# Kernel tuning notes

Measured on AMD Instinct MI355X. Metric: run time of the kernel, lower is better.

The kernel has to match this reference:

```python
import jax, jax.numpy as jnp
import numpy as np

NUM_EMB = 1000
HIDDEN = 256
SCALE = 2
N_HEADS = 8
HEAD_DIM = HIDDEN * SCALE // N_HEADS  # 64
HS = HIDDEN * SCALE  # 512
EPS = 1e-6


def setup_inputs() -> dict:
    key = jax.random.key(0)
    ks = jax.random.split(key, 12)
    B, N, C, H, W = 8, 8, HIDDEN, 32, 32
    std = 0.02
    return {
        "q": jax.random.randint(ks[0], (B,), 0, NUM_EMB, dtype=jnp.int32),
        "c": jax.random.normal(ks[1], (B, N, C, H, W), dtype=jnp.float32),
        "rms_w": jnp.ones((HIDDEN,), dtype=jnp.float32),
        "emb": jax.random.normal(ks[2], (NUM_EMB, HIDDEN), dtype=jnp.float32) * std,
        "w1": jax.random.normal(ks[3], (HIDDEN, HS), dtype=jnp.float32) * std,
        "b1": jnp.zeros((HS,), dtype=jnp.float32),
        "w2": jax.random.normal(ks[4], (HS, HS), dtype=jnp.float32) * std,
        "b2": jnp.zeros((HS,), dtype=jnp.float32),
        "w_kv": jax.random.normal(ks[5], (HIDDEN, HS * 2), dtype=jnp.float32) * std,
        "w_out": jax.random.normal(ks[6], (HS, HIDDEN), dtype=jnp.float32) * std,
        "b_out": jnp.zeros((HIDDEN,), dtype=jnp.float32),
    }


def reference(q, c, rms_w, emb, w1, b1, w2, b2, w_kv, w_out, b_out):
    B, N, C, H, W = c.shape
    attn_scale = HEAD_DIM ** (-0.5)
    # permute to [B,H,W,N,C] and RMSNorm over channel dim
    c = jnp.transpose(c, (0, 3, 4, 1, 2))
    c = c * jax.lax.rsqrt(jnp.mean(c * c, axis=-1, keepdims=True) + EPS) * rms_w
    # query path: embed + gated MLP -> [B, n_heads, head_dim]
    qe = emb[q]                                   # [B, hidden]
    qh = jax.nn.silu(qe @ w1 + b1) @ w2 + b2      # [B, HS]
    qh = qh.reshape(B, N_HEADS, HEAD_DIM)
    # kv projection: [B,H,W,N, 2*HS] -> [B,H,W,n_heads,N, 2*head_dim]
    kv = (c @ w_kv).reshape(B, H, W, N, N_HEADS, 2 * HEAD_DIM)
    kv = jnp.transpose(kv, (0, 1, 2, 4, 3, 5))
    k, v = jnp.split(kv, 2, axis=-1)              # each [B,H,W,heads,N,head_dim]
    # broadcast per-pixel cross-attention: query shared over H,W
    dots = jnp.einsum('bed,bhwend->bhwen', qh, k) * attn_scale
    attn = jax.nn.softmax(dots, axis=-1)
    h = jnp.einsum('bhwen,bhwend->bhwed', attn, v)  # [B,H,W,heads,head_dim]
    h = h.reshape(B, H, W, HS)
    out = h @ w_out + b_out                        # [B,H,W,hidden]
    return jnp.transpose(out, (0, 3, 1, 2))        # [B,hidden,H,W]
```

## Files before the change

### kernel.cpp

```cpp
#include <hip/hip_runtime.h>

typedef _Float16 f16;
typedef _Float16 f16x4 __attribute__((ext_vector_type(4)));
typedef _Float16 f16x8 __attribute__((ext_vector_type(8)));
typedef float f32x4 __attribute__((ext_vector_type(4)));

static __device__ inline char* a_addr(char* Abase, int px, int k) {
    return Abase + px * 4096 + ((((k >> 3) ^ (px & 15)) << 4) | ((k & 7) << 1));
}

__launch_bounds__(256)
__global__ void k_setup(const int* __restrict__ q, const float* __restrict__ emb,
                        const float* __restrict__ w1, const float* __restrict__ b1,
                        const float* __restrict__ w2, const float* __restrict__ b2,
                        const float* __restrict__ w_kv, const float* __restrict__ w_out,
                        const float* __restrict__ rms_w,
                        f16* __restrict__ qkw, f16* __restrict__ mtp) {
    int blk = blockIdx.x;
    int t = threadIdx.x;
    __shared__ float qe[256];
    __shared__ float x1L[512];
    __shared__ float ps[4][64];
    __shared__ float qhL[64];
    __shared__ float wv[64][8];

    if (blk < 64) {
        int b = blk >> 3, e = blk & 7;
        qe[t] = emb[(size_t)q[b] * 256 + t];
        __syncthreads();
        float a0 = b1[t], a1 = b1[t + 256];
#pragma unroll 4
        for (int c = 0; c < 256; ++c) {
            float qv = qe[c];
            a0 += qv * w1[c * 512 + t];
            a1 += qv * w1[c * 512 + t + 256];
        }
        x1L[t]       = a0 / (1.f + __expf(-a0));
        x1L[t + 256] = a1 / (1.f + __expf(-a1));
        __syncthreads();
        int d = t & 63, ks = t >> 6;
        float acc = 0.f;
#pragma unroll 4
        for (int k = ks * 128; k < ks * 128 + 128; ++k)
            acc += x1L[k] * w2[k * 512 + e * 64 + d];
        ps[ks][d] = acc;
        __syncthreads();
        if (t < 64)
            qhL[t] = b2[e * 64 + t] + ps[0][t] + ps[1][t] + ps[2][t] + ps[3][t];
        __syncthreads();
        const float* row = w_kv + (size_t)t * 1024 + e * 128;
        float a2 = 0.f;
#pragma unroll
        for (int dd = 0; dd < 64; dd += 4) {
            float4 wv4 = *(const float4*)(row + dd);
            a2 += qhL[dd] * wv4.x + qhL[dd + 1] * wv4.y + qhL[dd + 2] * wv4.z + qhL[dd + 3] * wv4.w;
        }
        qkw[(b * 8 + e) * 256 + t] = (f16)(a2 * rms_w[t]);
    } else {
        int mb = blk - 64;
        int e = mb >> 5, c0 = (mb & 31) * 8;
        {
            int d = t & 63, cc = t >> 6;
            wv[d][cc]     = w_kv[(size_t)(c0 + cc) * 1024 + e * 128 + 64 + d];
            wv[d][cc + 4] = w_kv[(size_t)(c0 + cc + 4) * 1024 + e * 128 + 64 + d];
        }
        __syncthreads();
        int o = t;
        float acc[8];
#pragma unroll
        for (int c = 0; c < 8; ++c) acc[c] = 0.f;
#pragma unroll 4
        for (int d = 0; d < 64; ++d) {
            float wo = w_out[(size_t)(e * 64 + d) * 256 + o];
            float4 wa = *(const float4*)&wv[d][0];
            float4 wb = *(const float4*)&wv[d][4];
            acc[0] += wa.x * wo; acc[1] += wa.y * wo; acc[2] += wa.z * wo; acc[3] += wa.w * wo;
            acc[4] += wb.x * wo; acc[5] += wb.y * wo; acc[6] += wb.z * wo; acc[7] += wb.w * wo;
        }
        f16x8 ov;
#pragma unroll
        for (int c = 0; c < 8; ++c) ov[c] = (f16)(acc[c] * rms_w[c0 + c]);
        *(f16x8*)(mtp + ((size_t)((e * 256 + c0) >> 3) * 256 + o) * 8) = ov;
    }
}

__launch_bounds__(1024, 8)
__global__ void k_attn(const float* __restrict__ cin, const f16* __restrict__ qkw,
                       const f16* __restrict__ mtp, const float* __restrict__ b_out,
                       float* __restrict__ out) {
    int blk = blockIdx.x;
    int b = blk & 7;
    int hw0 = (blk >> 3) * 16;
    int t = threadIdx.x;
    int lane = t & 63, w = t >> 6;
    int m16 = lane & 15, quad = lane >> 4;

    __shared__ char A[16 * 4096];
    __shared__ float dotsP[8][8][16];
    __shared__ float wred[16][16];
    __shared__ float rinvL[16][9];

    {
        int px = m16;
        int cb = (w << 2) | quad;
        const float* src = cin + ((size_t)b * 2048 + (size_t)cb * 32) * 1024 + hw0 + px;
        float ss = 0.f;
#pragma unroll
        for (int jb = 0; jb < 4; jb += 2) {
            float v0[8], v1[8];
#pragma unroll
            for (int j = 0; j < 8; ++j) v0[j] = src[(size_t)(jb * 8 + j) << 10];
#pragma unroll
            for (int j = 0; j < 8; ++j) v1[j] = src[(size_t)(jb * 8 + 8 + j) << 10];
            f16x8 h0, h1;
#pragma unroll
            for (int j = 0; j < 8; ++j) { ss += v0[j] * v0[j]; h0[j] = (f16)v0[j]; }
#pragma unroll
            for (int j = 0; j < 8; ++j) { ss += v1[j] * v1[j]; h1[j] = (f16)v1[j]; }
            *(f16x8*)a_addr(A, px, cb * 32 + jb * 8)     = h0;
            *(f16x8*)a_addr(A, px, cb * 32 + jb * 8 + 8) = h1;
        }
        ss += __shfl_xor(ss, 16);
        ss += __shfl_xor(ss, 32);
        if (lane < 16) wred[w][lane] = ss;
    }
    __syncthreads();

    if (w < 8) {
        int n = w;
        f32x4 d0 = {0.f, 0.f, 0.f, 0.f};
        const f16* qrow = qkw + (size_t)b * 2048 + (m16 & 7) * 256;
#pragma unroll
        for (int ks = 0; ks < 8; ++ks) {
            f16x8 a0 = *(const f16x8*)a_addr(A, m16, n * 256 + ks * 32 + quad * 8);
            f16x8 bq = *(const f16x8*)(qrow + ks * 32 + quad * 8);
            d0 = __builtin_amdgcn_mfma_f32_16x16x32_f16(a0, bq, d0, 0, 0, 0);
        }
        if (m16 < 8) {
#pragma unroll
            for (int r = 0; r < 4; ++r) dotsP[n][m16][quad * 4 + r] = d0[r];
        }
    } else if (w < 10) {
        int i = t - 512;
        int p = i & 15, n = i >> 4;
        float ss = wred[2 * n][p] + wred[2 * n + 1][p];
        rinvL[p][n] = rsqrtf(ss * (1.f / 256.f) + 1e-6f);
    }
    __syncthreads();

    {
        int bpx = t & 15;
        int cw = t >> 4;
        float rinv[8];
#pragma unroll
        for (int n = 0; n < 8; ++n) rinv[n] = rinvL[bpx][n];
        f16x4 cv[8];
#pragma unroll
        for (int n = 0; n < 8; ++n)
            cv[n] = *(const f16x4*)a_addr(A, bpx, n * 256 + cw * 4);
#pragma unroll
        for (int e = 0; e < 8; ++e) {
            float l[8];
#pragma unroll
            for (int n = 0; n < 8; ++n) l[n] = dotsP[n][e][bpx] * rinv[n] * 0.125f;
            float mx = l[0];
#pragma unroll
            for (int n = 1; n < 8; ++n) mx = fmaxf(mx, l[n]);
            float s = 0.f;
#pragma unroll
            for (int n = 0; n < 8; ++n) { l[n] = __expf(l[n] - mx); s += l[n]; }
            float inv = 1.f / s;
            f16x4 r = {};
#pragma unroll
            for (int n = 0; n < 8; ++n) {
                f16 an = (f16)(l[n] * inv * rinv[n]);
#pragma unroll
                for (int j = 0; j < 4; ++j) r[j] += cv[n][j] * an;
            }
            *(f16x4*)a_addr(A, bpx, e * 256 + cw * 4) = r;
        }
    }
    __syncthreads();

    {
        int o = (w << 4) | m16;
        float bo = b_out[o];
        f32x4 acc = {0.f, 0.f, 0.f, 0.f};
#pragma unroll 4
        for (int ks = 0; ks < 64; ++ks) {
            int k = ks * 32 + quad * 8;
            f16x8 bfr = *(const f16x8*)(mtp + ((size_t)(ks * 4 + quad) * 256 + o) * 8);
            f16x8 af  = *(const f16x8*)a_addr(A, m16, k);
            acc = __builtin_amdgcn_mfma_f32_16x16x32_f16(af, bfr, acc, 0, 0, 0);
        }
        float* drow = out + ((size_t)b * 256 + o) * 1024 + hw0;
        float4 v0 = {acc[0] + bo, acc[1] + bo, acc[2] + bo, acc[3] + bo};
        *(float4*)(drow + quad * 4) = v0;
    }
}

extern "C" void kernel_launch(void* const* d_in, const int* in_sizes, int n_in,
                              void* d_out, int out_size, void* d_ws, size_t ws_size,
                              hipStream_t stream) {
    (void)in_sizes; (void)n_in; (void)out_size; (void)ws_size;
    const int*   q     = (const int*)d_in[0];
    const float* c     = (const float*)d_in[1];
    const float* rms_w = (const float*)d_in[2];
    const float* emb   = (const float*)d_in[3];
    const float* w1    = (const float*)d_in[4];
    const float* b1    = (const float*)d_in[5];
    const float* w2    = (const float*)d_in[6];
    const float* b2    = (const float*)d_in[7];
    const float* w_kv  = (const float*)d_in[8];
    const float* w_out = (const float*)d_in[9];
    const float* b_out = (const float*)d_in[10];
    float* out = (float*)d_out;

    char* ws = (char*)d_ws;
    f16* qkw = (f16*)ws;
    f16* mtp = (f16*)(ws + 32768);

    k_setup<<<320, 256, 0, stream>>>(q, emb, w1, b1, w2, b2, w_kv, w_out, rms_w, qkw, mtp);
    k_attn <<<512, 1024, 0, stream>>>(c, qkw, mtp, b_out, out);
}
```

Baseline: 178.2 us.

## Process two pixel tiles per attention block and restructure setup kernel

```diff
diff --git a/kernel.cpp b/kernel.cpp
--- a/kernel.cpp
+++ b/kernel.cpp
@@ -9,7 +9,7 @@
     return Abase + px * 4096 + ((((k >> 3) ^ (px & 15)) << 4) | ((k & 7) << 1));
 }
 
-__launch_bounds__(256)
+__launch_bounds__(1024)
 __global__ void k_setup(const int* __restrict__ q, const float* __restrict__ emb,
                         const float* __restrict__ w1, const float* __restrict__ b1,
                         const float* __restrict__ w2, const float* __restrict__ b2,
@@ -18,64 +18,98 @@
                         f16* __restrict__ qkw, f16* __restrict__ mtp) {
     int blk = blockIdx.x;
     int t = threadIdx.x;
-    __shared__ float qe[256];
-    __shared__ float x1L[512];
-    __shared__ float ps[4][64];
-    __shared__ float qhL[64];
-    __shared__ float wv[64][8];
-
-    if (blk < 64) {
-        int b = blk >> 3, e = blk & 7;
-        qe[t] = emb[(size_t)q[b] * 256 + t];
-        __syncthreads();
-        float a0 = b1[t], a1 = b1[t + 256];
+
+    if (blk == 0) {
+        __shared__ float qeL[8][256];
+        __shared__ float x1L[8][512];
+        __shared__ float qhL[8][512];
+        {
+            int bb = t >> 8, c = t & 255;
+            qeL[bb][c]     = emb[(size_t)q[bb] * 256 + c];
+            qeL[bb + 4][c] = emb[(size_t)q[bb + 4] * 256 + c];
+        }
+        __syncthreads();
+        {
+            int bb = t >> 7, hq = t & 127;
+            float4 bv = *(const float4*)(b1 + hq * 4);
+            f32x4 acc = {bv.x, bv.y, bv.z, bv.w};
+#pragma unroll 8
+            for (int c = 0; c < 256; ++c) {
+                float4 wr = *(const float4*)(w1 + (size_t)c * 512 + hq * 4);
+                float qv = qeL[bb][c];
+                acc[0] += qv * wr.x; acc[1] += qv * wr.y;
+                acc[2] += qv * wr.z; acc[3] += qv * wr.w;
+            }
+#pragma unroll
+            for (int j = 0; j < 4; ++j) {
+                float a = acc[j];
+                x1L[bb][hq * 4 + j] = a / (1.f + __expf(-a));
+            }
+        }
+        __syncthreads();
+        {
+            int bb = t >> 7, oq = t & 127;
+            float4 bv = *(const float4*)(b2 + oq * 4);
+            f32x4 acc = {bv.x, bv.y, bv.z, bv.w};
+#pragma unroll 8
+            for (int k = 0; k < 512; ++k) {
+                float4 wr = *(const float4*)(w2 + (size_t)k * 512 + oq * 4);
+                float xv = x1L[bb][k];
+                acc[0] += xv * wr.x; acc[1] += xv * wr.y;
+                acc[2] += xv * wr.z; acc[3] += xv * wr.w;
+            }
+#pragma unroll
+            for (int j = 0; j < 4; ++j) qhL[bb][oq * 4 + j] = acc[j];
+        }
+        __syncthreads();
+        {
+            int c = t & 255;
+            float rw = rms_w[c];
+#pragma unroll
+            for (int e2 = 0; e2 < 2; ++e2) {
+                int e = (t >> 8) * 2 + e2;
+                const float* col = w_kv + (size_t)c * 1024 + e * 128;
+                float acc[8] = {0.f, 0.f, 0.f, 0.f, 0.f, 0.f, 0.f, 0.f};
 #pragma unroll 4
-        for (int c = 0; c < 256; ++c) {
-            float qv = qe[c];
-            a0 += qv * w1[c * 512 + t];
-            a1 += qv * w1[c * 512 + t + 256];
-        }
-        x1L[t]       = a0 / (1.f + __expf(-a0));
-        x1L[t + 256] = a1 / (1.f + __expf(-a1));
-        __syncthreads();
-        int d = t & 63, ks = t >> 6;
-        float acc = 0.f;
-#pragma unroll 4
-        for (int k = ks * 128; k < ks * 128 + 128; ++k)
-            acc += x1L[k] * w2[k * 512 + e * 64 + d];
-        ps[ks][d] = acc;
-        __syncthreads();
-        if (t < 64)
-            qhL[t] = b2[e * 64 + t] + ps[0][t] + ps[1][t] + ps[2][t] + ps[3][t];
-        __syncthreads();
-        const float* row = w_kv + (size_t)t * 1024 + e * 128;
-        float a2 = 0.f;
-#pragma unroll
-        for (int dd = 0; dd < 64; dd += 4) {
-            float4 wv4 = *(const float4*)(row + dd);
-            a2 += qhL[dd] * wv4.x + qhL[dd + 1] * wv4.y + qhL[dd + 2] * wv4.z + qhL[dd + 3] * wv4.w;
-        }
-        qkw[(b * 8 + e) * 256 + t] = (f16)(a2 * rms_w[t]);
+                for (int dq = 0; dq < 16; ++dq) {
+                    float4 wv4 = *(const float4*)(col + dq * 4);
+#pragma unroll
+                    for (int bb = 0; bb < 8; ++bb) {
+                        const float* qb = &qhL[bb][e * 64 + dq * 4];
+                        acc[bb] += wv4.x * qb[0] + wv4.y * qb[1]
+                                 + wv4.z * qb[2] + wv4.w * qb[3];
+                    }
+                }
+#pragma unroll
+                for (int bb = 0; bb < 8; ++bb)
+                    qkw[(bb * 8 + e) * 256 + c] = (f16)(acc[bb] * rw);
+            }
+        }
     } else {
-        int mb = blk - 64;
+        __shared__ float wv[4][64][8];
+        int sub = t >> 8, st = t & 255;
+        int mb = (blk - 1) * 4 + sub;
         int e = mb >> 5, c0 = (mb & 31) * 8;
-        {
-            int d = t & 63, cc = t >> 6;
-            wv[d][cc]     = w_kv[(size_t)(c0 + cc) * 1024 + e * 128 + 64 + d];
-            wv[d][cc + 4] = w_kv[(size_t)(c0 + cc + 4) * 1024 + e * 128 + 64 + d];
-        }
-        __syncthreads();
-        int o = t;
+        int o = st;
+        float wo[64];
+#pragma unroll
+        for (int d = 0; d < 64; ++d) wo[d] = w_out[(size_t)(e * 64 + d) * 256 + o];
+        {
+            int d = st & 63, cc = st >> 6;
+            wv[sub][d][cc]     = w_kv[(size_t)(c0 + cc) * 1024 + e * 128 + 64 + d];
+            wv[sub][d][cc + 4] = w_kv[(size_t)(c0 + cc + 4) * 1024 + e * 128 + 64 + d];
+        }
+        __syncthreads();
         float acc[8];
 #pragma unroll
         for (int c = 0; c < 8; ++c) acc[c] = 0.f;
-#pragma unroll 4
+#pragma unroll 8
         for (int d = 0; d < 64; ++d) {
-            float wo = w_out[(size_t)(e * 64 + d) * 256 + o];
-            float4 wa = *(const float4*)&wv[d][0];
-            float4 wb = *(const float4*)&wv[d][4];
-            acc[0] += wa.x * wo; acc[1] += wa.y * wo; acc[2] += wa.z * wo; acc[3] += wa.w * wo;
-            acc[4] += wb.x * wo; acc[5] += wb.y * wo; acc[6] += wb.z * wo; acc[7] += wb.w * wo;
+            float w = wo[d];
+            float4 wa = *(const float4*)&wv[sub][d][0];
+            float4 wb = *(const float4*)&wv[sub][d][4];
+            acc[0] += wa.x * w; acc[1] += wa.y * w; acc[2] += wa.z * w; acc[3] += wa.w * w;
+            acc[4] += wb.x * w; acc[5] += wb.y * w; acc[6] += wb.z * w; acc[7] += wb.w * w;
         }
         f16x8 ov;
 #pragma unroll
@@ -84,118 +118,154 @@
     }
 }
 
-__launch_bounds__(1024, 8)
+static __device__ inline void dots_rinv(char* A, const f16* qkw_b,
+                                        float (*dotsP)[8][16], float (*wred)[16],
+                                        float (*rinvL)[9],
+                                        int t, int w, int m16, int quad) {
+    if (w < 8) {
+        int n = w;
+        f32x4 d0 = {0.f, 0.f, 0.f, 0.f};
+        const f16* qrow = qkw_b + (m16 & 7) * 256;
+#pragma unroll
+        for (int ks = 0; ks < 8; ++ks) {
+            f16x8 a0 = *(const f16x8*)a_addr(A, m16, n * 256 + ks * 32 + quad * 8);
+            f16x8 bq = *(const f16x8*)(qrow + ks * 32 + quad * 8);
+            d0 = __builtin_amdgcn_mfma_f32_16x16x32_f16(a0, bq, d0, 0, 0, 0);
+        }
+        if (m16 < 8) {
+#pragma unroll
+            for (int r = 0; r < 4; ++r) dotsP[n][m16][quad * 4 + r] = d0[r];
+        }
+    } else if (w < 10) {
+        int i = t - 512;
+        int p = i & 15, n = i >> 4;
+        float ss = wred[2 * n][p] + wred[2 * n + 1][p];
+        rinvL[p][n] = rsqrtf(ss * (1.f / 256.f) + 1e-6f);
+    }
+}
+
+static __device__ inline void blend(char* A, float (*dotsP)[8][16],
+                                    float (*rinvL)[9], int t) {
+    int bpx = t & 15;
+    int cw = t >> 4;
+    float rinv[8];
+#pragma unroll
+    for (int n = 0; n < 8; ++n) rinv[n] = rinvL[bpx][n];
+    f16x4 cv[8];
+#pragma unroll
+    for (int n = 0; n < 8; ++n)
+        cv[n] = *(const f16x4*)a_addr(A, bpx, n * 256 + cw * 4);
+#pragma unroll
+    for (int e = 0; e < 8; ++e) {
+        float l[8];
+#pragma unroll
+        for (int n = 0; n < 8; ++n) l[n] = dotsP[n][e][bpx] * rinv[n] * 0.125f;
+        float mx = l[0];
+#pragma unroll
+        for (int n = 1; n < 8; ++n) mx = fmaxf(mx, l[n]);
+        float s = 0.f;
+#pragma unroll
+        for (int n = 0; n < 8; ++n) { l[n] = __expf(l[n] - mx); s += l[n]; }
+        float inv = 1.f / s;
+        f16x4 r = {};
+#pragma unroll
+        for (int n = 0; n < 8; ++n) {
+            f16 an = (f16)(l[n] * inv * rinv[n]);
+#pragma unroll
+            for (int j = 0; j < 4; ++j) r[j] += cv[n][j] * an;
+        }
+        *(f16x4*)a_addr(A, bpx, e * 256 + cw * 4) = r;
+    }
+}
+
+__launch_bounds__(1024, 4)
 __global__ void k_attn(const float* __restrict__ cin, const f16* __restrict__ qkw,
                        const f16* __restrict__ mtp, const float* __restrict__ b_out,
                        float* __restrict__ out) {
     int blk = blockIdx.x;
     int b = blk & 7;
-    int hw0 = (blk >> 3) * 16;
+    int hw0 = (blk >> 3) * 32;
     int t = threadIdx.x;
     int lane = t & 63, w = t >> 6;
     int m16 = lane & 15, quad = lane >> 4;
 
-    __shared__ char A[16 * 4096];
+    __shared__ char A0[16 * 4096];
+    __shared__ char A1[16 * 4096];
     __shared__ float dotsP[8][8][16];
     __shared__ float wred[16][16];
     __shared__ float rinvL[16][9];
 
+    int px = m16;
+    int cb = (w << 2) | quad;
+    const float* src0 = cin + ((size_t)b * 2048 + (size_t)cb * 32) * 1024 + hw0 + px;
+    const float* src1 = src0 + 16;
+
+    float v0[32], v1[32];
+#pragma unroll
+    for (int j = 0; j < 32; ++j) v0[j] = src0[(size_t)j << 10];
+    float ss0 = 0.f;
     {
-        int px = m16;
-        int cb = (w << 2) | quad;
-        const float* src = cin + ((size_t)b * 2048 + (size_t)cb * 32) * 1024 + hw0 + px;
-        float ss = 0.f;
-#pragma unroll
-        for (int jb = 0; jb < 4; jb += 2) {
-            float v0[8], v1[8];
-#pragma unroll
-            for (int j = 0; j < 8; ++j) v0[j] = src[(size_t)(jb * 8 + j) << 10];
-#pragma unroll
-            for (int j = 0; j < 8; ++j) v1[j] = src[(size_t)(jb * 8 + 8 + j) << 10];
-            f16x8 h0, h1;
-#pragma unroll
-            for (int j = 0; j < 8; ++j) { ss += v0[j] * v0[j]; h0[j] = (f16)v0[j]; }
-#pragma unroll
-            for (int j = 0; j < 8; ++j) { ss += v1[j] * v1[j]; h1[j] = (f16)v1[j]; }
-            *(f16x8*)a_addr(A, px, cb * 32 + jb * 8)     = h0;
-            *(f16x8*)a_addr(A, px, cb * 32 + jb * 8 + 8) = h1;
-        }
-        ss += __shfl_xor(ss, 16);
-        ss += __shfl_xor(ss, 32);
-        if (lane < 16) wred[w][lane] = ss;
-    }
-    __syncthreads();
-
-    if (w < 8) {
-        int n = w;
-        f32x4 d0 = {0.f, 0.f, 0.f, 0.f};
-        const f16* qrow = qkw + (size_t)b * 2048 + (m16 & 7) * 256;
-#pragma unroll
-        for (int ks = 0; ks < 8; ++ks) {
-            f16x8 a0 = *(const f16x8*)a_addr(A, m16, n * 256 + ks * 32 + quad * 8);
-            f16x8 bq = *(const f16x8*)(qrow + ks * 32 + quad * 8);
-            d0 = __builtin_amdgcn_mfma_f32_16x16x32_f16(a0, bq, d0, 0, 0, 0);
-        }
-        if (m16 < 8) {
-#pragma unroll
-            for (int r = 0; r < 4; ++r) dotsP[n][m16][quad * 4 + r] = d0[r];
-        }
-    } else if (w < 10) {
-        int i = t - 512;
-        int p = i & 15, n = i >> 4;
-        float ss = wred[2 * n][p] + wred[2 * n + 1][p];
-        rinvL[p][n] = rsqrtf(ss * (1.f / 256.f) + 1e-6f);
-    }
-    __syncthreads();
-
-    {
-        int bpx = t & 15;
-        int cw = t >> 4;
-        float rinv[8];
-#pragma unroll
-        for (int n = 0; n < 8; ++n) rinv[n] = rinvL[bpx][n];
-        f16x4 cv[8];
-#pragma unroll
-        for (int n = 0; n < 8; ++n)
-            cv[n] = *(const f16x4*)a_addr(A, bpx, n * 256 + cw * 4);
-#pragma unroll
-        for (int e = 0; e < 8; ++e) {
-            float l[8];
-#pragma unroll
-            for (int n = 0; n < 8; ++n) l[n] = dotsP[n][e][bpx] * rinv[n] * 0.125f;
-            float mx = l[0];
-#pragma unroll
-            for (int n = 1; n < 8; ++n) mx = fmaxf(mx, l[n]);
-            float s = 0.f;
-#pragma unroll
-            for (int n = 0; n < 8; ++n) { l[n] = __expf(l[n] - mx); s += l[n]; }
-            float inv = 1.f / s;
-            f16x4 r = {};
-#pragma unroll
-            for (int n = 0; n < 8; ++n) {
-                f16 an = (f16)(l[n] * inv * rinv[n]);
-#pragma unroll
-                for (int j = 0; j < 4; ++j) r[j] += cv[n][j] * an;
-            }
-            *(f16x4*)a_addr(A, bpx, e * 256 + cw * 4) = r;
-        }
-    }
+        f16x8 h;
+#pragma unroll
+        for (int j = 0; j < 8; ++j) { float x = v0[j]; ss0 += x * x; h[j] = (f16)x; }
+        *(f16x8*)a_addr(A0, px, cb * 32) = h;
+    }
+#pragma unroll
+    for (int j = 0; j < 32; ++j) v1[j] = src1[(size_t)j << 10];
+#pragma unroll
+    for (int g = 1; g < 4; ++g) {
+        f16x8 h;
+#pragma unroll
+        for (int j = 0; j < 8; ++j) { float x = v0[g * 8 + j]; ss0 += x * x; h[j] = (f16)x; }
+        *(f16x8*)a_addr(A0, px, cb * 32 + g * 8) = h;
+    }
+    ss0 += __shfl_xor(ss0, 16);
+    ss0 += __shfl_xor(ss0, 32);
+    if (lane < 16) wred[w][lane] = ss0;
+    __syncthreads();
+
+    dots_rinv(A0, qkw + (size_t)b * 2048, dotsP, wred, rinvL, t, w, m16, quad);
+    __syncthreads();
+    blend(A0, dotsP, rinvL, t);
+    __syncthreads();
+
+    float ss1 = 0.f;
+#pragma unroll
+    for (int g = 0; g < 4; ++g) {
+        f16x8 h;
+#pragma unroll
+        for (int j = 0; j < 8; ++j) { float x = v1[g * 8 + j]; ss1 += x * x; h[j] = (f16)x; }
+        *(f16x8*)a_addr(A1, px, cb * 32 + g * 8) = h;
+    }
+    ss1 += __shfl_xor(ss1, 16);
+    ss1 += __shfl_xor(ss1, 32);
+    if (lane < 16) wred[w][lane] = ss1;
+    __syncthreads();
+
+    dots_rinv(A1, qkw + (size_t)b * 2048, dotsP, wred, rinvL, t, w, m16, quad);
+    __syncthreads();
+    blend(A1, dotsP, rinvL, t);
     __syncthreads();
 
     {
         int o = (w << 4) | m16;
         float bo = b_out[o];
-        f32x4 acc = {0.f, 0.f, 0.f, 0.f};
-#pragma unroll 4
+        f32x4 acc0 = {0.f, 0.f, 0.f, 0.f};
+        f32x4 acc1 = {0.f, 0.f, 0.f, 0.f};
+#pragma unroll 8
         for (int ks = 0; ks < 64; ++ks) {
             int k = ks * 32 + quad * 8;
             f16x8 bfr = *(const f16x8*)(mtp + ((size_t)(ks * 4 + quad) * 256 + o) * 8);
-            f16x8 af  = *(const f16x8*)a_addr(A, m16, k);
-            acc = __builtin_amdgcn_mfma_f32_16x16x32_f16(af, bfr, acc, 0, 0, 0);
+            f16x8 af0 = *(const f16x8*)a_addr(A0, m16, k);
+            f16x8 af1 = *(const f16x8*)a_addr(A1, m16, k);
+            acc0 = __builtin_amdgcn_mfma_f32_16x16x32_f16(af0, bfr, acc0, 0, 0, 0);
+            acc1 = __builtin_amdgcn_mfma_f32_16x16x32_f16(af1, bfr, acc1, 0, 0, 0);
         }
         float* drow = out + ((size_t)b * 256 + o) * 1024 + hw0;
-        float4 v0 = {acc[0] + bo, acc[1] + bo, acc[2] + bo, acc[3] + bo};
-        *(float4*)(drow + quad * 4) = v0;
+        float4 r0 = {acc0[0] + bo, acc0[1] + bo, acc0[2] + bo, acc0[3] + bo};
+        float4 r1 = {acc1[0] + bo, acc1[1] + bo, acc1[2] + bo, acc1[3] + bo};
+        *(float4*)(drow + quad * 4)      = r0;
+        *(float4*)(drow + 16 + quad * 4) = r1;
     }
 }
 
@@ -220,6 +290,6 @@
     f16* qkw = (f16*)ws;
     f16* mtp = (f16*)(ws + 32768);
 
-    k_setup<<<320, 256, 0, stream>>>(q, emb, w1, b1, w2, b2, w_kv, w_out, rms_w, qkw, mtp);
-    k_attn <<<512, 1024, 0, stream>>>(c, qkw, mtp, b_out, out);
-}
+    k_setup<<<65, 1024, 0, stream>>>(q, emb, w1, b1, w2, b2, w_kv, w_out, rms_w, qkw, mtp);
+    k_attn <<<256, 1024, 0, stream>>>(c, qkw, mtp, b_out, out);
+}
```

New measurement: 285.7 us. 60.4% more time.

## Process two 16-pixel tiles per block, prefetching second tile during first

Applied to the files above, without the earlier changes.

```diff
diff --git a/kernel.cpp b/kernel.cpp
--- a/kernel.cpp
+++ b/kernel.cpp
@@ -84,118 +84,154 @@
     }
 }
 
-__launch_bounds__(1024, 8)
+static __device__ inline void dots_rinv(char* A, const f16* qkw_b,
+                                        float (*dotsP)[8][16], float (*wred)[16],
+                                        float (*rinvL)[9],
+                                        int t, int w, int m16, int quad) {
+    if (w < 8) {
+        int n = w;
+        f32x4 d0 = {0.f, 0.f, 0.f, 0.f};
+        const f16* qrow = qkw_b + (m16 & 7) * 256;
+#pragma unroll
+        for (int ks = 0; ks < 8; ++ks) {
+            f16x8 a0 = *(const f16x8*)a_addr(A, m16, n * 256 + ks * 32 + quad * 8);
+            f16x8 bq = *(const f16x8*)(qrow + ks * 32 + quad * 8);
+            d0 = __builtin_amdgcn_mfma_f32_16x16x32_f16(a0, bq, d0, 0, 0, 0);
+        }
+        if (m16 < 8) {
+#pragma unroll
+            for (int r = 0; r < 4; ++r) dotsP[n][m16][quad * 4 + r] = d0[r];
+        }
+    } else if (w < 10) {
+        int i = t - 512;
+        int p = i & 15, n = i >> 4;
+        float ss = wred[2 * n][p] + wred[2 * n + 1][p];
+        rinvL[p][n] = rsqrtf(ss * (1.f / 256.f) + 1e-6f);
+    }
+}
+
+static __device__ inline void blend(char* A, float (*dotsP)[8][16],
+                                    float (*rinvL)[9], int t) {
+    int bpx = t & 15;
+    int cw = t >> 4;
+    float rinv[8];
+#pragma unroll
+    for (int n = 0; n < 8; ++n) rinv[n] = rinvL[bpx][n];
+    f16x4 cv[8];
+#pragma unroll
+    for (int n = 0; n < 8; ++n)
+        cv[n] = *(const f16x4*)a_addr(A, bpx, n * 256 + cw * 4);
+#pragma unroll
+    for (int e = 0; e < 8; ++e) {
+        float l[8];
+#pragma unroll
+        for (int n = 0; n < 8; ++n) l[n] = dotsP[n][e][bpx] * rinv[n] * 0.125f;
+        float mx = l[0];
+#pragma unroll
+        for (int n = 1; n < 8; ++n) mx = fmaxf(mx, l[n]);
+        float s = 0.f;
+#pragma unroll
+        for (int n = 0; n < 8; ++n) { l[n] = __expf(l[n] - mx); s += l[n]; }
+        float inv = 1.f / s;
+        f16x4 r = {};
+#pragma unroll
+        for (int n = 0; n < 8; ++n) {
+            f16 an = (f16)(l[n] * inv * rinv[n]);
+#pragma unroll
+            for (int j = 0; j < 4; ++j) r[j] += cv[n][j] * an;
+        }
+        *(f16x4*)a_addr(A, bpx, e * 256 + cw * 4) = r;
+    }
+}
+
+__launch_bounds__(1024, 4)
 __global__ void k_attn(const float* __restrict__ cin, const f16* __restrict__ qkw,
                        const f16* __restrict__ mtp, const float* __restrict__ b_out,
                        float* __restrict__ out) {
     int blk = blockIdx.x;
     int b = blk & 7;
-    int hw0 = (blk >> 3) * 16;
+    int hw0 = (blk >> 3) * 32;
     int t = threadIdx.x;
     int lane = t & 63, w = t >> 6;
     int m16 = lane & 15, quad = lane >> 4;
 
-    __shared__ char A[16 * 4096];
+    __shared__ char A0[16 * 4096];
+    __shared__ char A1[16 * 4096];
     __shared__ float dotsP[8][8][16];
     __shared__ float wred[16][16];
     __shared__ float rinvL[16][9];
 
+    int px = m16;
+    int cb = (w << 2) | quad;
+    const float* src0 = cin + ((size_t)b * 2048 + (size_t)cb * 32) * 1024 + hw0 + px;
+    const float* src1 = src0 + 16;
+
+    float v0[32], v1[32];
+#pragma unroll
+    for (int j = 0; j < 32; ++j) v0[j] = src0[(size_t)j << 10];
+    float ss0 = 0.f;
     {
-        int px = m16;
-        int cb = (w << 2) | quad;
-        const float* src = cin + ((size_t)b * 2048 + (size_t)cb * 32) * 1024 + hw0 + px;
-        float ss = 0.f;
-#pragma unroll
-        for (int jb = 0; jb < 4; jb += 2) {
-            float v0[8], v1[8];
-#pragma unroll
-            for (int j = 0; j < 8; ++j) v0[j] = src[(size_t)(jb * 8 + j) << 10];
-#pragma unroll
-            for (int j = 0; j < 8; ++j) v1[j] = src[(size_t)(jb * 8 + 8 + j) << 10];
-            f16x8 h0, h1;
-#pragma unroll
-            for (int j = 0; j < 8; ++j) { ss += v0[j] * v0[j]; h0[j] = (f16)v0[j]; }
-#pragma unroll
-            for (int j = 0; j < 8; ++j) { ss += v1[j] * v1[j]; h1[j] = (f16)v1[j]; }
-            *(f16x8*)a_addr(A, px, cb * 32 + jb * 8)     = h0;
-            *(f16x8*)a_addr(A, px, cb * 32 + jb * 8 + 8) = h1;
-        }
-        ss += __shfl_xor(ss, 16);
-        ss += __shfl_xor(ss, 32);
-        if (lane < 16) wred[w][lane] = ss;
-    }
-    __syncthreads();
-
-    if (w < 8) {
-        int n = w;
-        f32x4 d0 = {0.f, 0.f, 0.f, 0.f};
-        const f16* qrow = qkw + (size_t)b * 2048 + (m16 & 7) * 256;
-#pragma unroll
-        for (int ks = 0; ks < 8; ++ks) {
-            f16x8 a0 = *(const f16x8*)a_addr(A, m16, n * 256 + ks * 32 + quad * 8);
-            f16x8 bq = *(const f16x8*)(qrow + ks * 32 + quad * 8);
-            d0 = __builtin_amdgcn_mfma_f32_16x16x32_f16(a0, bq, d0, 0, 0, 0);
-        }
-        if (m16 < 8) {
-#pragma unroll
-            for (int r = 0; r < 4; ++r) dotsP[n][m16][quad * 4 + r] = d0[r];
-        }
-    } else if (w < 10) {
-        int i = t - 512;
-        int p = i & 15, n = i >> 4;
-        float ss = wred[2 * n][p] + wred[2 * n + 1][p];
-        rinvL[p][n] = rsqrtf(ss * (1.f / 256.f) + 1e-6f);
-    }
-    __syncthreads();
-
-    {
-        int bpx = t & 15;
-        int cw = t >> 4;
-        float rinv[8];
-#pragma unroll
-        for (int n = 0; n < 8; ++n) rinv[n] = rinvL[bpx][n];
-        f16x4 cv[8];
-#pragma unroll
-        for (int n = 0; n < 8; ++n)
-            cv[n] = *(const f16x4*)a_addr(A, bpx, n * 256 + cw * 4);
-#pragma unroll
-        for (int e = 0; e < 8; ++e) {
-            float l[8];
-#pragma unroll
-            for (int n = 0; n < 8; ++n) l[n] = dotsP[n][e][bpx] * rinv[n] * 0.125f;
-            float mx = l[0];
-#pragma unroll
-            for (int n = 1; n < 8; ++n) mx = fmaxf(mx, l[n]);
-            float s = 0.f;
-#pragma unroll
-            for (int n = 0; n < 8; ++n) { l[n] = __expf(l[n] - mx); s += l[n]; }
-            float inv = 1.f / s;
-            f16x4 r = {};
-#pragma unroll
-            for (int n = 0; n < 8; ++n) {
-                f16 an = (f16)(l[n] * inv * rinv[n]);
-#pragma unroll
-                for (int j = 0; j < 4; ++j) r[j] += cv[n][j] * an;
-            }
-            *(f16x4*)a_addr(A, bpx, e * 256 + cw * 4) = r;
-        }
-    }
+        f16x8 h;
+#pragma unroll
+        for (int j = 0; j < 8; ++j) { float x = v0[j]; ss0 += x * x; h[j] = (f16)x; }
+        *(f16x8*)a_addr(A0, px, cb * 32) = h;
+    }
+#pragma unroll
+    for (int j = 0; j < 32; ++j) v1[j] = src1[(size_t)j << 10];
+#pragma unroll
+    for (int g = 1; g < 4; ++g) {
+        f16x8 h;
+#pragma unroll
+        for (int j = 0; j < 8; ++j) { float x = v0[g * 8 + j]; ss0 += x * x; h[j] = (f16)x; }
+        *(f16x8*)a_addr(A0, px, cb * 32 + g * 8) = h;
+    }
+    ss0 += __shfl_xor(ss0, 16);
+    ss0 += __shfl_xor(ss0, 32);
+    if (lane < 16) wred[w][lane] = ss0;
+    __syncthreads();
+
+    dots_rinv(A0, qkw + (size_t)b * 2048, dotsP, wred, rinvL, t, w, m16, quad);
+    __syncthreads();
+    blend(A0, dotsP, rinvL, t);
+    __syncthreads();
+
+    float ss1 = 0.f;
+#pragma unroll
+    for (int g = 0; g < 4; ++g) {
+        f16x8 h;
+#pragma unroll
+        for (int j = 0; j < 8; ++j) { float x = v1[g * 8 + j]; ss1 += x * x; h[j] = (f16)x; }
+        *(f16x8*)a_addr(A1, px, cb * 32 + g * 8) = h;
+    }
+    ss1 += __shfl_xor(ss1, 16);
+    ss1 += __shfl_xor(ss1, 32);
+    if (lane < 16) wred[w][lane] = ss1;
+    __syncthreads();
+
+    dots_rinv(A1, qkw + (size_t)b * 2048, dotsP, wred, rinvL, t, w, m16, quad);
+    __syncthreads();
+    blend(A1, dotsP, rinvL, t);
     __syncthreads();
 
     {
         int o = (w << 4) | m16;
         float bo = b_out[o];
-        f32x4 acc = {0.f, 0.f, 0.f, 0.f};
-#pragma unroll 4
+        f32x4 acc0 = {0.f, 0.f, 0.f, 0.f};
+        f32x4 acc1 = {0.f, 0.f, 0.f, 0.f};
+#pragma unroll 8
         for (int ks = 0; ks < 64; ++ks) {
             int k = ks * 32 + quad * 8;
             f16x8 bfr = *(const f16x8*)(mtp + ((size_t)(ks * 4 + quad) * 256 + o) * 8);
-            f16x8 af  = *(const f16x8*)a_addr(A, m16, k);
-            acc = __builtin_amdgcn_mfma_f32_16x16x32_f16(af, bfr, acc, 0, 0, 0);
+            f16x8 af0 = *(const f16x8*)a_addr(A0, m16, k);
+            f16x8 af1 = *(const f16x8*)a_addr(A1, m16, k);
+            acc0 = __builtin_amdgcn_mfma_f32_16x16x32_f16(af0, bfr, acc0, 0, 0, 0);
+            acc1 = __builtin_amdgcn_mfma_f32_16x16x32_f16(af1, bfr, acc1, 0, 0, 0);
         }
         float* drow = out + ((size_t)b * 256 + o) * 1024 + hw0;
-        float4 v0 = {acc[0] + bo, acc[1] + bo, acc[2] + bo, acc[3] + bo};
-        *(float4*)(drow + quad * 4) = v0;
+        float4 r0 = {acc0[0] + bo, acc0[1] + bo, acc0[2] + bo, acc0[3] + bo};
+        float4 r1 = {acc1[0] + bo, acc1[1] + bo, acc1[2] + bo, acc1[3] + bo};
+        *(float4*)(drow + quad * 4)      = r0;
+        *(float4*)(drow + 16 + quad * 4) = r1;
     }
 }
 
@@ -221,5 +257,5 @@
     f16* mtp = (f16*)(ws + 32768);
 
     k_setup<<<320, 256, 0, stream>>>(q, emb, w1, b1, w2, b2, w_kv, w_out, rms_w, qkw, mtp);
-    k_attn <<<512, 1024, 0, stream>>>(c, qkw, mtp, b_out, out);
-}
+    k_attn <<<256, 1024, 0, stream>>>(c, qkw, mtp, b_out, out);
+}
```

After: 176.0 us. Within noise of the previous version (-1.2%).
